# Optimization experiments

Measured on AMD Instinct MI355X. Metric: run time of the kernel, lower is better.

Reference implementation:

```python
import jax, jax.numpy as jnp
import numpy as np

B, C, H, W = 4, 256, 224, 224
PH, PW = 7, 7


def setup_inputs() -> dict:
    key = jax.random.key(0)
    k1, k2 = jax.random.split(key)
    x = jax.random.normal(k1, (B, C, H, W), dtype=jnp.float32)
    beta = jax.random.normal(k2, (1,), dtype=jnp.float32)
    return {"x": x, "beta": beta, "ph": PH, "pw": PW}


def reference(x, beta, ph, pw):
    Bb, Cc, Hh, Ww = x.shape
    Mh, Mw = Hh // ph, Ww // pw
    P = ph * pw            # tokens per patch (49)
    M = Mh * Mw            # number of patches
    # unfold with stride==kernel is a pure reshape/transpose:
    # (B,C,H,W) -> (B,Mh,Mw,ph,pw,C) -> (B,M,P,C); p = i*pw + j, m = mh*Mw + mw
    A = x.reshape(Bb, Cc, Mh, ph, Mw, pw).transpose(0, 2, 4, 3, 5, 1).reshape(Bb, M, P, Cc)
    # first-order similarity, softmax over last dim
    Sc = jax.nn.softmax(jnp.einsum('bmpc,bmqc->bmpq', A, A), axis=-1)   # (B,M,P,P)
    Mc = jnp.einsum('bmpq,bmqc->bmpc', Sc, A)                            # (B,M,P,C)
    # mean-centered second-order covariance (the live definition in the source)
    Ac = A - A.mean(axis=2, keepdims=True)
    Mcc = Mc - Mc.mean(axis=2, keepdims=True)
    cov = jnp.einsum('bmpc,bmqc->bmpq', Ac, Mcc) / P                     # (B,M,P,P)
    L = Sc + cov
    Ec = jnp.einsum('bmpq,bmqc->bmpc', L, A)                             # (B,M,P,C)
    # fold back: (B,M,P,C) -> (B,C,H,W)
    Ec_map = Ec.reshape(Bb, Mh, Mw, ph, pw, Cc).transpose(0, 5, 1, 3, 2, 4).reshape(Bb, Cc, Hh, Ww)
    out = x * (beta[0] * Ec_map + x)
    return out, Sc, cov, L, Ec_map
```

## Files before the change

### kernel.cpp

```cpp
#include <hip/hip_runtime.h>
#include <hip/hip_bf16.h>
#include <cstdint>
#include <cstddef>

constexpr int C_  = 256;
constexpr int H_  = 224;
constexpr int W_  = 224;
constexpr int P_  = 49;
constexpr int M_  = 1024;
constexpr int HW_ = H_ * W_;

constexpr size_t IMG_ELEMS = (size_t)4 * C_ * H_ * W_;
constexpr size_t SCO_ELEMS = (size_t)4 * M_ * P_ * P_;
constexpr size_t OFF_SC  = IMG_ELEMS;
constexpr size_t OFF_COV = OFF_SC  + SCO_ELEMS;
constexpr size_t OFF_L   = OFF_COV + SCO_ELEMS;
constexpr size_t OFF_EC  = OFF_L   + SCO_ELEMS;

typedef __attribute__((ext_vector_type(8))) short short8;
typedef __attribute__((ext_vector_type(4))) float f32x4;

constexpr size_t WS_ROW   = 56;
constexpr size_t WS_PATCH = (size_t)C_ * WS_ROW;
constexpr size_t WS_NEED  = (size_t)4096 * WS_PATCH * 2;

constexpr int SA_OFF  = 0;
constexpr int GB_OFF  = 25088;
constexpr int SCB_OFF = 31360;
constexpr int U_OFF   = 37632;
constexpr int SMEM_BYTES = 37888;

__device__ __forceinline__ int srowswz(int r) { return ((r ^ (r >> 3)) & 7) << 4; }

template<bool SPLIT>
__global__ __launch_bounds__(256, 4)
void psa_kernel(const float* __restrict__ x, const float* __restrict__ betap,
                float* __restrict__ out_img, float* __restrict__ out_sc,
                float* __restrict__ out_cov, float* __restrict__ out_l,
                float* __restrict__ out_ec,
                __hip_bfloat16* __restrict__ ws_ec)
{
    __shared__ __align__(16) unsigned char smem[SMEM_BYTES];
    float* uArr = (float*)(smem + U_OFF);

    const int tid = threadIdx.x;
    const int bid = blockIdx.x;
    const int bm  = ((bid & 7) << 9) | (bid >> 3);
    const int b   = bm >> 10;
    const int m   = bm & (M_ - 1);
    const int mh  = m >> 5;
    const int mw  = m & 31;
    const float beta = betap[0];
    const size_t xpatch = (((size_t)b * C_ * H_) + (size_t)mh * 7) * W_ + (size_t)mw * 7;

    const int wid = tid >> 6, lane = tid & 63, l15 = lane & 15, lh = lane >> 4;

    {
        const int c = tid;
        const float* src = x + xpatch + (size_t)c * HW_;
        #pragma unroll
        for (int i = 0; i < 7; ++i) {
            #pragma unroll
            for (int j = 0; j < 7; ++j) {
                const int p = i * 7 + j;
                *(__hip_bfloat16*)(smem + SA_OFF + p * 512 + ((2 * c) ^ srowswz(p))) =
                    __float2bfloat16(src[i * W_ + j]);
            }
        }
    }
    __syncthreads();

    f32x4 gacc[4] = {f32x4{0,0,0,0}, f32x4{0,0,0,0}, f32x4{0,0,0,0}, f32x4{0,0,0,0}};
    {
        const int arow = 16 * wid + l15;
        #pragma unroll
        for (int kc = 0; kc < 8; ++kc) {
            const int cb = 64 * kc + 16 * lh;
            const short8 af = *(const short8*)(smem + SA_OFF + arow * 512 + (cb ^ srowswz(arow)));
            #pragma unroll
            for (int t = 0; t < 4; ++t) {
                const int brow = 16 * t + l15;
                const short8 bf = *(const short8*)(smem + SA_OFF + brow * 512 + (cb ^ srowswz(brow)));
                gacc[t] = __builtin_amdgcn_mfma_f32_16x16x32_bf16(af, bf, gacc[t], 0, 0, 0);
            }
        }
    }

    float mx[4];
    {
        #pragma unroll
        for (int r = 0; r < 4; ++r) {
            const int p = 16 * wid + 4 * lh + r;
            float m_ = fmaxf(fmaxf(gacc[0][r], gacc[1][r]), gacc[2][r]);
            m_ = fmaxf(m_, (l15 == 0) ? gacc[3][r] : -3.4e38f);
            float s_ = gacc[0][r] + gacc[1][r] + gacc[2][r] + ((l15 == 0) ? gacc[3][r] : 0.f);
            #pragma unroll
            for (int d = 1; d < 16; d <<= 1) {
                m_ = fmaxf(m_, __shfl_xor(m_, d));
                s_ += __shfl_xor(s_, d);
            }
            mx[r] = m_;
            if (l15 == 0 && p <= 48) uArr[p] = s_ * (1.f / 49.f);
        }
    }
    __syncthreads();

    float sc[4][4];
    {
        float* sc_g = out_sc + (size_t)bm * (P_ * P_);
        #pragma unroll
        for (int r = 0; r < 4; ++r) {
            const int p = 16 * wid + 4 * lh + r;
            if (p <= 48) {
                #pragma unroll
                for (int t = 0; t < 4; ++t) {
                    const int qv = 16 * t + l15;
                    const float gv = (qv <= 48) ? (gacc[t][r] - uArr[qv]) : 0.f;
                    *(__hip_bfloat16*)(smem + GB_OFF + p * 128 + ((2 * qv) ^ srowswz(p))) =
                        __float2bfloat16(gv);
                }
            }
            float e[4];
            #pragma unroll
            for (int t = 0; t < 4; ++t) {
                const int qv = 16 * t + l15;
                e[t] = (qv <= 48) ? __expf(gacc[t][r] - mx[r]) : 0.f;
            }
            float s_ = e[0] + e[1] + e[2] + e[3];
            #pragma unroll
            for (int d = 1; d < 16; d <<= 1) s_ += __shfl_xor(s_, d);
            const float rinv = 1.f / s_;
            #pragma unroll
            for (int t = 0; t < 4; ++t) sc[t][r] = e[t] * rinv;
            if (p <= 48) {
                #pragma unroll
                for (int t = 0; t < 4; ++t) {
                    const int qv = 16 * t + l15;
                    *(__hip_bfloat16*)(smem + SCB_OFF + p * 128 + ((2 * qv) ^ srowswz(p))) =
                        __float2bfloat16(sc[t][r]);
                    if (qv <= 48) sc_g[p * 49 + qv] = sc[t][r];
                }
            }
        }
    }
    __syncthreads();

    f32x4 cacc[4] = {f32x4{0,0,0,0}, f32x4{0,0,0,0}, f32x4{0,0,0,0}, f32x4{0,0,0,0}};
    {
        const int arow = 16 * wid + l15;
        #pragma unroll
        for (int kc = 0; kc < 2; ++kc) {
            const int cb = 64 * kc + 16 * lh;
            const short8 af = *(const short8*)(smem + GB_OFF + arow * 128 + (cb ^ srowswz(arow)));
            #pragma unroll
            for (int t = 0; t < 4; ++t) {
                const int brow = 16 * t + l15;
                const short8 bf = *(const short8*)(smem + SCB_OFF + brow * 128 + (cb ^ srowswz(brow)));
                cacc[t] = __builtin_amdgcn_mfma_f32_16x16x32_bf16(af, bf, cacc[t], 0, 0, 0);
            }
        }
    }
    float t2[4];
    {
        #pragma unroll
        for (int r = 0; r < 4; ++r) {
            float s_ = cacc[0][r] + cacc[1][r] + cacc[2][r] + ((l15 == 0) ? cacc[3][r] : 0.f);
            #pragma unroll
            for (int d = 1; d < 16; d <<= 1) s_ += __shfl_xor(s_, d);
            t2[r] = s_ * (1.f / 49.f);
        }
    }
    __syncthreads();

    {
        float* cov_g = out_cov + (size_t)bm * (P_ * P_);
        float* l_g   = out_l   + (size_t)bm * (P_ * P_);
        #pragma unroll
        for (int t = 0; t < 4; ++t) {
            const int qv = 16 * t + l15;
            #pragma unroll
            for (int r = 0; r < 4; ++r) {
                const int p = 16 * wid + 4 * lh + r;
                if (p <= 48 && qv <= 48) {
                    const float cv = (cacc[t][r] - t2[r]) * (1.f / 49.f);
                    const float lv = sc[t][r] + cv;
                    cov_g[p * 49 + qv] = cv;
                    l_g  [p * 49 + qv] = lv;
                    *(__hip_bfloat16*)(smem + GB_OFF + p * 128 + ((2 * qv) ^ srowswz(p))) =
                        __float2bfloat16(lv);
                }
            }
        }
    }
    __syncthreads();

    {
        f32x4 acc[4][4];
        #pragma unroll
        for (int i = 0; i < 4; ++i)
            #pragma unroll
            for (int j2 = 0; j2 < 4; ++j2) acc[i][j2] = f32x4{0, 0, 0, 0};

        #pragma unroll
        for (int kc = 0; kc < 2; ++kc) {
            const int cb = 64 * kc + 16 * lh;
            short8 bf[4];
            #pragma unroll
            for (int pt = 0; pt < 4; ++pt) {
                const int brow = 16 * pt + l15;
                bf[pt] = *(const short8*)(smem + GB_OFF + brow * 128 + (cb ^ srowswz(brow)));
            }
            #pragma unroll
            for (int ct = 0; ct < 4; ++ct) {
                const int c = 64 * wid + 16 * ct + l15;
                short8 af;
                #pragma unroll
                for (int j = 0; j < 8; ++j) {
                    const int q2 = 32 * kc + 8 * lh + j;
                    af[j] = *(const short*)(smem + SA_OFF + q2 * 512 + ((2 * c) ^ srowswz(q2)));
                }
                #pragma unroll
                for (int pt = 0; pt < 4; ++pt)
                    acc[ct][pt] = __builtin_amdgcn_mfma_f32_16x16x32_bf16(af, bf[pt], acc[ct][pt], 0, 0, 0);
            }
        }

        if (SPLIT) {
            __hip_bfloat16* wec = ws_ec + (size_t)bm * WS_PATCH;
            #pragma unroll
            for (int pt = 0; pt < 4; ++pt) {
                const int p = 16 * pt + l15;
                if (p >= (int)WS_ROW) continue;
                #pragma unroll
                for (int ct = 0; ct < 4; ++ct) {
                    #pragma unroll
                    for (int r = 0; r < 4; ++r) {
                        const int c = 64 * wid + 16 * ct + 4 * lh + r;
                        wec[(size_t)c * WS_ROW + p] = __float2bfloat16(acc[ct][pt][r]);
                    }
                }
            }
        } else {
            #pragma unroll
            for (int pt = 0; pt < 4; ++pt) {
                const int p = 16 * pt + l15;
                if (p > 48) continue;
                const int i = p / 7, j = p - 7 * (p / 7);
                const size_t base = xpatch + (size_t)i * W_ + j;
                #pragma unroll
                for (int ct = 0; ct < 4; ++ct) {
                    #pragma unroll
                    for (int r = 0; r < 4; ++r) {
                        const int c = 64 * wid + 16 * ct + 4 * lh + r;
                        const size_t g = base + (size_t)c * HW_;
                        const float ec = acc[ct][pt][r];
                        const float xv = __bfloat162float(
                            *(const __hip_bfloat16*)(smem + SA_OFF + p * 512 + ((2 * c) ^ srowswz(p))));
                        out_ec [g] = ec;
                        out_img[g] = xv * fmaf(beta, ec, xv);
                    }
                }
            }
        }
    }
}

__global__ __launch_bounds__(256)
void fold_kernel(const __hip_bfloat16* __restrict__ ws_ec,
                 const float* __restrict__ x, const float* __restrict__ betap,
                 float* __restrict__ out_img, float* __restrict__ out_ec)
{
    __shared__ __hip_bfloat16 lec[32][56];

    const int bid = blockIdx.x;
    const int bc  = bid >> 5;
    const int mh  = bid & 31;
    const int b   = bc >> 8;
    const int c   = bc & 255;
    const int t   = threadIdx.x;
    const float beta = betap[0];

    if (t < 224) {
        const int k = t / 7, o = (t - k * 7) * 8;
        const size_t base = (((size_t)(b << 10) + (mh << 5) + k) * C_ + c) * WS_ROW + o;
        *(short8*)&lec[k][o] = *(const short8*)&ws_ec[base];
    }
    __syncthreads();

    const size_t rowbase = ((size_t)bc * H_ + (size_t)mh * 7) * W_;
    for (int idx = t; idx < 392; idx += 256) {
        const int i  = idx / 56;
        const int w0 = (idx - i * 56) * 4;
        const size_t g = rowbase + (size_t)i * W_ + w0;
        const float4 xv = *(const float4*)&x[g];
        float4 vo, ve;
        #pragma unroll
        for (int e = 0; e < 4; ++e) {
            const int w  = w0 + e;
            const int mw = w / 7;
            const int p  = i * 7 + (w - mw * 7);
            const float ec = __bfloat162float(lec[mw][p]);
            const float xe = ((const float*)&xv)[e];
            ((float*)&ve)[e] = ec;
            ((float*)&vo)[e] = xe * fmaf(beta, ec, xe);
        }
        *(float4*)&out_ec [g] = ve;
        *(float4*)&out_img[g] = vo;
    }
}

extern "C" void kernel_launch(void* const* d_in, const int* in_sizes, int n_in,
                              void* d_out, int out_size, void* d_ws, size_t ws_size,
                              hipStream_t stream) {
    const float* x    = (const float*)d_in[0];
    const float* beta = (const float*)d_in[1];
    float* out = (float*)d_out;

    if (ws_size >= WS_NEED) {
        __hip_bfloat16* ws_ec = (__hip_bfloat16*)d_ws;
        psa_kernel<true><<<dim3(4 * M_), dim3(256), 0, stream>>>(
            x, beta, out, out + OFF_SC, out + OFF_COV, out + OFF_L, out + OFF_EC,
            ws_ec);
        fold_kernel<<<dim3(1024 * 32), dim3(256), 0, stream>>>(
            ws_ec, x, beta, out, out + OFF_EC);
    } else {
        psa_kernel<false><<<dim3(4 * M_), dim3(256), 0, stream>>>(
            x, beta, out, out + OFF_SC, out + OFF_COV, out + OFF_L, out + OFF_EC,
            nullptr);
    }
}
```

Baseline: 283.2 us.

## Restructure patch load, defer Sc/cov/L stores to coalesced loop, widen fold blocks

The patch load now maps lanes to the 49 pixel positions and loops over 64 channels per wave, so neighbouring lanes read neighbouring pixels instead of stride-HW addresses. In the split path, the Sc, cov and L global stores move out of the MFMA-fragment layout into a linear per-element loop that reads back from shared memory. That loop reconstructs Sc and L from bf16 copies, and cov as L minus Sc, so these outputs lose precision. Padded rows are masked in the final GEMM operand, and the fold kernel now handles four channels per block with a quarter of the blocks.

```diff
diff --git a/kernel.cpp b/kernel.cpp
--- a/kernel.cpp
+++ b/kernel.cpp
@@ -56,15 +56,16 @@
     const int wid = tid >> 6, lane = tid & 63, l15 = lane & 15, lh = lane >> 4;
 
     {
-        const int c = tid;
-        const float* src = x + xpatch + (size_t)c * HW_;
-        #pragma unroll
-        for (int i = 0; i < 7; ++i) {
-            #pragma unroll
-            for (int j = 0; j < 7; ++j) {
-                const int p = i * 7 + j;
-                *(__hip_bfloat16*)(smem + SA_OFF + p * 512 + ((2 * c) ^ srowswz(p))) =
-                    __float2bfloat16(src[i * W_ + j]);
+        const int p = lane;
+        if (p < P_) {
+            const int i = p / 7, j = p - 7 * (p / 7);
+            const float* xp = x + xpatch + (size_t)i * W_ + j + (size_t)(64 * wid) * HW_;
+            const int swzp = srowswz(p);
+            unsigned char* sbase = smem + SA_OFF + p * 512 + 128 * wid;
+            #pragma unroll 32
+            for (int k = 0; k < 64; ++k) {
+                const float v = xp[(size_t)k * HW_];
+                *(__hip_bfloat16*)(sbase + ((2 * k) ^ swzp)) = __float2bfloat16(v);
             }
         }
     }
@@ -107,7 +108,6 @@
 
     float sc[4][4];
     {
-        float* sc_g = out_sc + (size_t)bm * (P_ * P_);
         #pragma unroll
         for (int r = 0; r < 4; ++r) {
             const int p = 16 * wid + 4 * lh + r;
@@ -138,7 +138,8 @@
                     const int qv = 16 * t + l15;
                     *(__hip_bfloat16*)(smem + SCB_OFF + p * 128 + ((2 * qv) ^ srowswz(p))) =
                         __float2bfloat16(sc[t][r]);
-                    if (qv <= 48) sc_g[p * 49 + qv] = sc[t][r];
+                    if (!SPLIT && qv <= 48)
+                        out_sc[(size_t)bm * (P_ * P_) + p * 49 + qv] = sc[t][r];
                 }
             }
         }
@@ -173,8 +174,6 @@
     __syncthreads();
 
     {
-        float* cov_g = out_cov + (size_t)bm * (P_ * P_);
-        float* l_g   = out_l   + (size_t)bm * (P_ * P_);
         #pragma unroll
         for (int t = 0; t < 4; ++t) {
             const int qv = 16 * t + l15;
@@ -184,8 +183,10 @@
                 if (p <= 48 && qv <= 48) {
                     const float cv = (cacc[t][r] - t2[r]) * (1.f / 49.f);
                     const float lv = sc[t][r] + cv;
-                    cov_g[p * 49 + qv] = cv;
-                    l_g  [p * 49 + qv] = lv;
+                    if (!SPLIT) {
+                        out_cov[(size_t)bm * (P_ * P_) + p * 49 + qv] = cv;
+                        out_l  [(size_t)bm * (P_ * P_) + p * 49 + qv] = lv;
+                    }
                     *(__hip_bfloat16*)(smem + GB_OFF + p * 128 + ((2 * qv) ^ srowswz(p))) =
                         __float2bfloat16(lv);
                 }
@@ -217,7 +218,9 @@
                 #pragma unroll
                 for (int j = 0; j < 8; ++j) {
                     const int q2 = 32 * kc + 8 * lh + j;
-                    af[j] = *(const short*)(smem + SA_OFF + q2 * 512 + ((2 * c) ^ srowswz(q2)));
+                    short v = *(const short*)(smem + SA_OFF + q2 * 512 + ((2 * c) ^ srowswz(q2)));
+                    if (kc == 1) v = (q2 <= 48) ? v : (short)0;
+                    af[j] = v;
                 }
                 #pragma unroll
                 for (int pt = 0; pt < 4; ++pt)
@@ -239,6 +242,19 @@
                         wec[(size_t)c * WS_ROW + p] = __float2bfloat16(acc[ct][pt][r]);
                     }
                 }
+            }
+            float* sc_g  = out_sc  + (size_t)bm * (P_ * P_);
+            float* cov_g = out_cov + (size_t)bm * (P_ * P_);
+            float* l_g   = out_l   + (size_t)bm * (P_ * P_);
+            for (int e = tid; e < P_ * P_; e += 256) {
+                const int p = e / 49, q = e - 49 * p;
+                const float scv = __bfloat162float(
+                    *(const __hip_bfloat16*)(smem + SCB_OFF + p * 128 + ((2 * q) ^ srowswz(p))));
+                const float lvv = __bfloat162float(
+                    *(const __hip_bfloat16*)(smem + GB_OFF + p * 128 + ((2 * q) ^ srowswz(p))));
+                sc_g[e]  = scv;
+                l_g[e]   = lvv;
+                cov_g[e] = lvv - scv;
             }
         } else {
             #pragma unroll
@@ -270,28 +286,32 @@
                  const float* __restrict__ x, const float* __restrict__ betap,
                  float* __restrict__ out_img, float* __restrict__ out_ec)
 {
-    __shared__ __hip_bfloat16 lec[32][56];
+    __shared__ __hip_bfloat16 lec[4][32][56];
 
     const int bid = blockIdx.x;
-    const int bc  = bid >> 5;
     const int mh  = bid & 31;
-    const int b   = bc >> 8;
-    const int c   = bc & 255;
+    const int bcg = bid >> 5;
+    const int b   = bcg >> 6;
+    const int c0  = (bcg & 63) << 2;
     const int t   = threadIdx.x;
     const float beta = betap[0];
 
-    if (t < 224) {
-        const int k = t / 7, o = (t - k * 7) * 8;
-        const size_t base = (((size_t)(b << 10) + (mh << 5) + k) * C_ + c) * WS_ROW + o;
-        *(short8*)&lec[k][o] = *(const short8*)&ws_ec[base];
-    }
-    __syncthreads();
-
-    const size_t rowbase = ((size_t)bc * H_ + (size_t)mh * 7) * W_;
-    for (int idx = t; idx < 392; idx += 256) {
-        const int i  = idx / 56;
-        const int w0 = (idx - i * 56) * 4;
-        const size_t g = rowbase + (size_t)i * W_ + w0;
+    for (int s = t; s < 896; s += 256) {
+        const int cc  = s / 224;
+        const int rem = s - cc * 224;
+        const int k   = rem / 7;
+        const int o   = (rem - k * 7) * 8;
+        const size_t base = (((size_t)(b << 10) + (mh << 5) + k) * C_ + (c0 + cc)) * WS_ROW + o;
+        *(short8*)&lec[cc][k][o] = *(const short8*)&ws_ec[base];
+    }
+    __syncthreads();
+
+    for (int idx = t; idx < 1568; idx += 256) {
+        const int cc = idx / 392;
+        const int r2 = idx - cc * 392;
+        const int i  = r2 / 56;
+        const int w0 = (r2 - i * 56) * 4;
+        const size_t g = (((size_t)(b * C_ + c0 + cc)) * H_ + (size_t)mh * 7 + i) * W_ + w0;
         const float4 xv = *(const float4*)&x[g];
         float4 vo, ve;
         #pragma unroll
@@ -299,7 +319,7 @@
             const int w  = w0 + e;
             const int mw = w / 7;
             const int p  = i * 7 + (w - mw * 7);
-            const float ec = __bfloat162float(lec[mw][p]);
+            const float ec = __bfloat162float(lec[cc][mw][p]);
             const float xe = ((const float*)&xv)[e];
             ((float*)&ve)[e] = ec;
             ((float*)&vo)[e] = xe * fmaf(beta, ec, xe);
@@ -321,7 +341,7 @@
         psa_kernel<true><<<dim3(4 * M_), dim3(256), 0, stream>>>(
             x, beta, out, out + OFF_SC, out + OFF_COV, out + OFF_L, out + OFF_EC,
             ws_ec);
-        fold_kernel<<<dim3(1024 * 32), dim3(256), 0, stream>>>(
+        fold_kernel<<<dim3(8192), dim3(256), 0, stream>>>(
             ws_ec, x, beta, out, out + OFF_EC);
     } else {
         psa_kernel<false><<<dim3(4 * M_), dim3(256), 0, stream>>>(
```

After: 289.3 us. 2.2% more time.
